# Performance work log

Measured on AMD Instinct MI355X. Metric: run time of the kernel, lower is better.

The kernel has to match this reference:

```python
import jax, jax.numpy as jnp
from jax import lax
import numpy as np

NEG_INF = -10000.0
MAX_W = 15          # max_span_width for every marker
M = 5               # num_markers
H = 1024            # encoder hidden size (deberta-v3-large)
B, N = 16, 2048


def _gelu(x):
    return jax.nn.gelu(x, approximate=False)  # torch nn.GELU default (erf)


def _consistency(scores, mask, gamma, width_logits):
    # scores: [B, N] token scores for one marker; mask: [B, N] int
    n = scores.shape[1]
    masked = jnp.where(mask == 0, NEG_INF, scores)
    ww = jax.nn.softmax(width_logits)  # [MAX_W]
    boosts = [masked]
    for w in range(2, min(MAX_W, n) + 1):
        # sliding-window min of width w -> span_mins [B, n-w+1]
        mins = lax.reduce_window(masked, float('inf'), lax.min,
                                 (1, w), (1, 1), 'VALID')
        weighted = mins * ww[w - 2]
        # expand each span-min back to every token it covers via sliding max
        p = jnp.pad(weighted, ((0, 0), (w - 1, w - 1)), constant_values=NEG_INF)
        expanded = lax.reduce_window(p, float('-inf'), lax.max,
                                     (1, w), (1, 1), 'VALID')  # [B, n]
        boosts.append(expanded)
    boost = jnp.max(jnp.stack(boosts, axis=0), axis=0)
    return scores + gamma * boost


def setup_inputs() -> dict:
    key = jax.random.key(0)
    ks = jax.random.split(key, 12)
    s = 0.02
    inp = {
        'h': jax.random.normal(ks[0], (B, N, H), jnp.float32),
        'attention_mask': jnp.ones((B, N), jnp.int32),
        # per-marker token scorers, stacked on leading marker axis
        'W1': jax.random.normal(ks[1], (M, H, 512), jnp.float32) * s,
        'b1': jnp.zeros((M, 512), jnp.float32),
        'W2': jax.random.normal(ks[2], (M, 512, 256), jnp.float32) * s,
        'b2': jnp.zeros((M, 256), jnp.float32),
        'W3': jax.random.normal(ks[3], (M, 256), jnp.float32) * s,
        'b3': jnp.zeros((M,), jnp.float32),
        # span-consistency params
        'gamma': jnp.ones((M,), jnp.float32),
        'width_logits': jax.random.normal(ks[4], (M, MAX_W), jnp.float32) * 0.1,
        # cross-marker attention params
        'corr': jnp.eye(M, dtype=jnp.float32) * 0.5,
        'cw1': jax.random.normal(ks[5], (M, 64), jnp.float32) * 0.1,
        'cb1': jnp.zeros((64,), jnp.float32),
        'cw2': jax.random.normal(ks[6], (64, M), jnp.float32) * 0.1,
        'cb2': jnp.zeros((M,), jnp.float32),
        'gate': jnp.array(0.3, jnp.float32),
    }
    return inp


def reference(h, attention_mask, W1, b1, W2, b2, W3, b3,
              gamma, width_logits, corr, cw1, cb1, cw2, cb2, gate):
    # token scorers (dropout is identity in eval): [M, B, N]
    t1 = _gelu(jnp.einsum('bnh,mhd->mbnd', h, W1) + b1[:, None, None, :])
    t2 = _gelu(jnp.einsum('mbnd,mde->mbne', t1, W2) + b2[:, None, None, :])
    scores = jnp.einsum('mbne,me->mbn', t2, W3) + b3[:, None, None]
    # per-marker span-consistency boost
    boosted = jax.vmap(_consistency, in_axes=(0, None, 0, 0))(
        scores, attention_mask, gamma, width_logits)      # [M, B, N]
    logits = jnp.transpose(boosted, (1, 2, 0))            # [B, N, M]
    # cross-marker attention
    probs = jax.nn.sigmoid(logits)
    correlated = probs @ corr
    refined = _gelu(correlated @ cw1 + cb1) @ cw2 + cb2
    return logits + jax.nn.sigmoid(gate) * refined
```

## Files before the change

kernel.cpp:

```cpp
#include <hip/hip_runtime.h>
#include <math.h>


typedef __bf16 bf16x8 __attribute__((ext_vector_type(8)));
typedef float f32x4 __attribute__((ext_vector_type(4)));

#define NEG_INF_VAL (-10000.0f)

__device__ __forceinline__ unsigned short f2bf(float f) {
  union { float f; unsigned u; } v; v.f = f;
  unsigned r = v.u + 0x7fffu + ((v.u >> 16) & 1u);
  return (unsigned short)(r >> 16);
}
__device__ __forceinline__ float bf2f(unsigned short b) {
  union { unsigned u; float f; } v; v.u = ((unsigned)b) << 16;
  return v.f;
}
__device__ __forceinline__ float gelu_erf(float x) {
  return 0.5f * x * (1.0f + erff(x * 0.7071067811865476f));
}
__device__ __forceinline__ float gelu_fast(float x) {
  float u = 0.7978845608f * x * (1.0f + 0.044715f * x * x);
  float e = __expf(-2.0f * fabsf(u));
  float t = (1.0f - e) / (1.0f + e);
  t = copysignf(t, u);
  return 0.5f * x * (1.0f + t);
}

__global__ __launch_bounds__(256) void k_f32_to_bf16x4(
    const float* __restrict__ in, unsigned short* __restrict__ out, int n4) {
  int i = blockIdx.x * 256 + threadIdx.x;
  if (i >= n4) return;
  float4 v = reinterpret_cast<const float4*>(in)[i];
  ushort4 o;
  o.x = f2bf(v.x); o.y = f2bf(v.y); o.z = f2bf(v.z); o.w = f2bf(v.w);
  reinterpret_cast<ushort4*>(out)[i] = o;
}

__global__ __launch_bounds__(256) void k_transpose_tiled(
    const float* __restrict__ W, unsigned short* __restrict__ Wt,
    int K, int C) {
  __shared__ float tile[32][33];
  const int m = blockIdx.z;
  const int c0 = blockIdx.x * 32, k0 = blockIdx.y * 32;
  const int tx = threadIdx.x & 31, ty = threadIdx.x >> 5;
  const float* Wm = W + (size_t)m * K * C;
#pragma unroll
  for (int r = ty; r < 32; r += 8)
    tile[r][tx] = Wm[(size_t)(k0 + r) * C + c0 + tx];
  __syncthreads();
  unsigned short* Wtm = Wt + (size_t)m * C * K;
#pragma unroll
  for (int r = ty; r < 32; r += 8)
    Wtm[(size_t)(c0 + r) * K + k0 + tx] = f2bf(tile[tx][r]);
}

#define STAGE(GP, LP)                                                        \
  __builtin_amdgcn_global_load_lds(                                          \
      (const __attribute__((address_space(1))) void*)(GP),                   \
      (__attribute__((address_space(3))) void*)(LP), 16, 0, 0)

#define TILE(SLOT, DO_S1, DO_S0, VM1, VM3)                                   \
  {                                                                          \
    bf16x8 af[4], bfr[4];                                                    \
                                               \
    _Pragma("unroll") for (int j = 0; j < 4; ++j)                            \
      bfr[j] = *reinterpret_cast<const bf16x8*>(                             \
          &Bs[SLOT][(wc * 4 + j) * 1024 + l8]);                              \
    _Pragma("unroll") for (int i = 0; i < 4; ++i)                            \
      af[i] = *reinterpret_cast<const bf16x8*>(                              \
          &As[SLOT][(wr * 8 + i) * 1024 + l8]);                              \
    if (DO_S1) {                                                             \
      STAGE(pA0 + 96, &As[1 - (SLOT)][(0 * 8 + w) * 1024 + 512 + l8]);       \
      STAGE(pA1 + 96, &As[1 - (SLOT)][(1 * 8 + w) * 1024 + 512 + l8]);       \
    }                                                                        \
    __builtin_amdgcn_s_barrier();                                            \
    __builtin_amdgcn_sched_barrier(0);                                       \
    asm volatile("s_waitcnt lgkmcnt(0)" ::: "memory");                       \
    __builtin_amdgcn_sched_barrier(0);                                       \
    __builtin_amdgcn_s_setprio(1);                                           \
    _Pragma("unroll") for (int i = 0; i < 4; ++i)                            \
      _Pragma("unroll") for (int j = 0; j < 4; ++j)                          \
        acc[i][j] = __builtin_amdgcn_mfma_f32_16x16x32_bf16(                 \
            af[i], bfr[j], acc[i][j], 0, 0, 0);                              \
    __builtin_amdgcn_s_setprio(0);                                           \
    __builtin_amdgcn_sched_barrier(0);                                       \
    __builtin_amdgcn_s_barrier();                                            \
    __builtin_amdgcn_sched_barrier(0);                                       \
                                               \
    _Pragma("unroll") for (int i = 0; i < 4; ++i)                            \
      af[i] = *reinterpret_cast<const bf16x8*>(                              \
          &As[SLOT][(wr * 8 + 4 + i) * 1024 + l8]);                          \
    if (DO_S1) {                                                             \
      STAGE(pB0 + 96, &Bs[1 - (SLOT)][(0 * 8 + w) * 1024 + 512 + l8]);       \
      STAGE(pB1 + 96, &Bs[1 - (SLOT)][(1 * 8 + w) * 1024 + 512 + l8]);       \
    }                                                                        \
    __builtin_amdgcn_s_barrier();                                            \
    __builtin_amdgcn_sched_barrier(0);                                       \
    asm volatile("s_waitcnt lgkmcnt(0)" ::: "memory");                       \
    __builtin_amdgcn_sched_barrier(0);                                       \
    __builtin_amdgcn_s_setprio(1);                                           \
    _Pragma("unroll") for (int i = 0; i < 4; ++i)                            \
      _Pragma("unroll") for (int j = 0; j < 4; ++j)                          \
        acc[4 + i][j] = __builtin_amdgcn_mfma_f32_16x16x32_bf16(             \
            af[i], bfr[j], acc[4 + i][j], 0, 0, 0);                          \
    __builtin_amdgcn_s_setprio(0);                                           \
    __builtin_amdgcn_sched_barrier(0);                                       \
    asm volatile("s_waitcnt vmcnt(" VM1 ")" ::: "memory");                   \
    __builtin_amdgcn_sched_barrier(0);                                       \
    __builtin_amdgcn_s_barrier();                                            \
    __builtin_amdgcn_sched_barrier(0);                                       \
                                               \
    _Pragma("unroll") for (int j = 0; j < 4; ++j)                            \
      bfr[j] = *reinterpret_cast<const bf16x8*>(                             \
          &Bs[SLOT][(wc * 4 + j) * 1024 + 512 + l8]);                        \
    _Pragma("unroll") for (int i = 0; i < 4; ++i)                            \
      af[i] = *reinterpret_cast<const bf16x8*>(                              \
          &As[SLOT][(wr * 8 + i) * 1024 + 512 + l8]);                        \
    if (DO_S0) {                                                             \
      STAGE(pA0 + 128, &As[SLOT][(0 * 8 + w) * 1024 + l8]);                  \
      STAGE(pA1 + 128, &As[SLOT][(1 * 8 + w) * 1024 + l8]);                  \
    }                                                                        \
    __builtin_amdgcn_s_barrier();                                            \
    __builtin_amdgcn_sched_barrier(0);                                       \
    asm volatile("s_waitcnt lgkmcnt(0)" ::: "memory");                       \
    __builtin_amdgcn_sched_barrier(0);                                       \
    __builtin_amdgcn_s_setprio(1);                                           \
    _Pragma("unroll") for (int i = 0; i < 4; ++i)                            \
      _Pragma("unroll") for (int j = 0; j < 4; ++j)                          \
        acc[i][j] = __builtin_amdgcn_mfma_f32_16x16x32_bf16(                 \
            af[i], bfr[j], acc[i][j], 0, 0, 0);                              \
    __builtin_amdgcn_s_setprio(0);                                           \
    __builtin_amdgcn_sched_barrier(0);                                       \
    __builtin_amdgcn_s_barrier();                                            \
    __builtin_amdgcn_sched_barrier(0);                                       \
                                               \
    _Pragma("unroll") for (int i = 0; i < 4; ++i)                            \
      af[i] = *reinterpret_cast<const bf16x8*>(                              \
          &As[SLOT][(wr * 8 + 4 + i) * 1024 + 512 + l8]);                    \
    if (DO_S0) {                                                             \
      STAGE(pB0 + 128, &Bs[SLOT][(0 * 8 + w) * 1024 + l8]);                  \
      STAGE(pB1 + 128, &Bs[SLOT][(1 * 8 + w) * 1024 + l8]);                  \
    }                                                                        \
    __builtin_amdgcn_s_barrier();                                            \
    __builtin_amdgcn_sched_barrier(0);                                       \
    asm volatile("s_waitcnt lgkmcnt(0)" ::: "memory");                       \
    __builtin_amdgcn_sched_barrier(0);                                       \
    __builtin_amdgcn_s_setprio(1);                                           \
    _Pragma("unroll") for (int i = 0; i < 4; ++i)                            \
      _Pragma("unroll") for (int j = 0; j < 4; ++j)                          \
        acc[4 + i][j] = __builtin_amdgcn_mfma_f32_16x16x32_bf16(             \
            af[i], bfr[j], acc[4 + i][j], 0, 0, 0);                          \
    __builtin_amdgcn_s_setprio(0);                                           \
    __builtin_amdgcn_sched_barrier(0);                                       \
    asm volatile("s_waitcnt vmcnt(" VM3 ")" ::: "memory");                   \
    __builtin_amdgcn_sched_barrier(0);                                       \
    __builtin_amdgcn_s_barrier();                                            \
    __builtin_amdgcn_sched_barrier(0);                                       \
    pA0 += 64; pA1 += 64; pB0 += 64; pB1 += 64;                              \
  }

template <bool FUSE_SCORES, int NT>
__global__ __launch_bounds__(512) void k_gemm256(
    const unsigned short* __restrict__ A, int lda, int aOffPerM,
    const unsigned short* __restrict__ Bt, int K,
    const float* __restrict__ bias,
    unsigned short* __restrict__ C, int ldc,
    const float* __restrict__ W3, const float* __restrict__ b3,
    float* __restrict__ scoresOut,
    int tilesPerM, int colsPerM, int nColTiles) {
  __shared__ __align__(16) unsigned short As[2][16384];
  __shared__ __align__(16) unsigned short Bs[2][16384];
  __shared__ float sc[256];
  const int t512 = threadIdx.x;
  const int w = t512 >> 6, l = t512 & 63;
  const int wr = w >> 2, wc = w & 3;
  const int l8 = l * 8;

  const int nwg = gridDim.x;
  const int cpx = nwg >> 3;
  const int bid = blockIdx.x;
  const int swz = (bid & 7) * cpx + (bid >> 3);
  const int ct = swz % nColTiles, rt = swz / nColTiles;
  const int m = ct / tilesPerM, cb = ct - m * tilesPerM;
  const int gcol0 = m * colsPerM + cb * 256;
  const int row0 = rt * 256;
  const unsigned short* Am = A + (size_t)m * aOffPerM;

  if (FUSE_SCORES && t512 < 256) sc[t512] = 0.f;

  f32x4 acc[8][4] = {};

  const int r = l & 15;
  const int c8 = (l >> 4) * 8;
  const unsigned short* pA0 = Am + (size_t)(row0 + w * 16 + r) * lda + c8;
  const unsigned short* pA1 = Am + (size_t)(row0 + 128 + w * 16 + r) * lda + c8;
  const unsigned short* pB0 = Bt + (size_t)(gcol0 + w * 16 + r) * (size_t)K + c8;
  const unsigned short* pB1 = Bt + (size_t)(gcol0 + 128 + w * 16 + r) * (size_t)K + c8;

  STAGE(pA0,      &As[0][(0 * 8 + w) * 1024 + l8]);
  STAGE(pA1,      &As[0][(1 * 8 + w) * 1024 + l8]);
  STAGE(pB0,      &Bs[0][(0 * 8 + w) * 1024 + l8]);
  STAGE(pB1,      &Bs[0][(1 * 8 + w) * 1024 + l8]);
  STAGE(pA0 + 32, &As[0][(0 * 8 + w) * 1024 + 512 + l8]);
  STAGE(pA1 + 32, &As[0][(1 * 8 + w) * 1024 + 512 + l8]);
  STAGE(pB0 + 32, &Bs[0][(0 * 8 + w) * 1024 + 512 + l8]);
  STAGE(pB1 + 32, &Bs[0][(1 * 8 + w) * 1024 + 512 + l8]);
  STAGE(pA0 + 64, &As[1][(0 * 8 + w) * 1024 + l8]);
  STAGE(pA1 + 64, &As[1][(1 * 8 + w) * 1024 + l8]);
  STAGE(pB0 + 64, &Bs[1][(0 * 8 + w) * 1024 + l8]);
  STAGE(pB1 + 64, &Bs[1][(1 * 8 + w) * 1024 + l8]);
  asm volatile("s_waitcnt vmcnt(8)" ::: "memory");
  __builtin_amdgcn_sched_barrier(0);
  __builtin_amdgcn_s_barrier();
  __builtin_amdgcn_sched_barrier(0);

#pragma unroll 1
  for (int t = 0; t < NT - 2; t += 2) {
    TILE(0, 1, 1, "8", "8");
    TILE(1, 1, 1, "8", "8");
  }
  TILE(0, 1, 0, "8", "4");
  TILE(1, 0, 0, "0", "0");

  if (!FUSE_SCORES) {
    const int orow = (l >> 4) * 4, ocol = l & 15;
#pragma unroll
    for (int i = 0; i < 8; ++i)
#pragma unroll
      for (int j = 0; j < 4; ++j) {
        const int gc = gcol0 + wc * 64 + j * 16 + ocol;
        const float bv = bias[gc];
        const int gr0 = row0 + wr * 128 + i * 16 + orow;
#pragma unroll
        for (int rr = 0; rr < 4; ++rr) {
          float v = gelu_fast(acc[i][j][rr] + bv);
          C[(size_t)(gr0 + rr) * ldc + gc] = f2bf(v);
        }
      }
  } else {
    const int ocol = l & 15;
#pragma unroll
    for (int i = 0; i < 8; ++i) {
      float rs[4] = {0.f, 0.f, 0.f, 0.f};
#pragma unroll
      for (int j = 0; j < 4; ++j) {
        const int cl = wc * 64 + j * 16 + ocol;
        const float bv = bias[m * 256 + cl];
        const float w3v = W3[m * 256 + cl];
#pragma unroll
        for (int rr = 0; rr < 4; ++rr)
          rs[rr] += gelu_fast(acc[i][j][rr] + bv) * w3v;
      }
#pragma unroll
      for (int s = 1; s < 16; s <<= 1)
#pragma unroll
        for (int rr = 0; rr < 4; ++rr)
          rs[rr] += __shfl_xor(rs[rr], s);
      if (ocol == 0) {
        const int lr0 = wr * 128 + i * 16 + (l >> 4) * 4;
#pragma unroll
        for (int rr = 0; rr < 4; ++rr)
          atomicAdd(&sc[lr0 + rr], rs[rr]);
      }
    }
    __syncthreads();
    if (t512 < 256)
      scoresOut[(size_t)m * 32768 + row0 + t512] = sc[t512] + b3[m];
  }
}

__global__ __launch_bounds__(256) void k_span(
    const float* __restrict__ scores,
    const int* __restrict__ mask,
    const float* __restrict__ gamma,
    const float* __restrict__ wlog,
    float* __restrict__ logits) {
  const int b = blockIdx.x, m = blockIdx.y;
  const int tid = threadIdx.x;
  __shared__ float masked[2048], mins[2048], boost[2048];
  __shared__ float ww[14];
  if (tid == 0) {
    float mx = -1e30f;
    for (int i = 0; i < 15; i++) mx = fmaxf(mx, wlog[m * 15 + i]);
    float e[15], sum = 0.f;
    for (int i = 0; i < 15; i++) { e[i] = expf(wlog[m * 15 + i] - mx); sum += e[i]; }
    for (int i = 0; i < 14; i++) ww[i] = e[i] / sum;
  }
  const float* srow = scores + ((size_t)m * 16 + b) * 2048;
  const int* mrow = mask + (size_t)b * 2048;
  for (int i = tid; i < 2048; i += 256) {
    float s = srow[i];
    float mk = (mrow[i] == 0) ? NEG_INF_VAL : s;
    masked[i] = mk; mins[i] = mk; boost[i] = mk;
  }
  __syncthreads();
  for (int w2 = 2; w2 <= 15; w2++) {
    for (int s = tid; s <= 2048 - w2; s += 256)
      mins[s] = fminf(mins[s], masked[s + w2 - 1]);
    __syncthreads();
    float c = ww[w2 - 2];
    for (int i = tid; i < 2048; i += 256) {
      int lo = i - w2 + 1; if (lo < 0) lo = 0;
      int hi = i; if (hi > 2048 - w2) hi = 2048 - w2;
      float mx = -1e30f;
      for (int s = lo; s <= hi; s++) mx = fmaxf(mx, mins[s]);
      boost[i] = fmaxf(boost[i], mx * c);
    }
    __syncthreads();
  }
  float g = gamma[m];
  for (int i = tid; i < 2048; i += 256)
    logits[((size_t)b * 2048 + i) * 5 + m] = srow[i] + g * boost[i];
}

__global__ __launch_bounds__(256) void k_cross(
    const float* __restrict__ logits, const float* __restrict__ corr,
    const float* __restrict__ cw1, const float* __restrict__ cb1,
    const float* __restrict__ cw2, const float* __restrict__ cb2,
    const float* __restrict__ gate, float* __restrict__ out) {
  __shared__ float s_corr[25], s_cw1[320], s_cb1[64], s_cw2[320], s_cb2[5];
  int tid = threadIdx.x;
  if (tid < 25) s_corr[tid] = corr[tid];
  if (tid < 64) s_cb1[tid] = cb1[tid];
  if (tid < 5)  s_cb2[tid] = cb2[tid];
  for (int i = tid; i < 320; i += 256) { s_cw1[i] = cw1[i]; s_cw2[i] = cw2[i]; }
  __syncthreads();
  int t = blockIdx.x * 256 + tid;
  float lg[5], pr[5];
#pragma unroll
  for (int m = 0; m < 5; m++) {
    lg[m] = logits[(size_t)t * 5 + m];
    pr[m] = 1.f / (1.f + expf(-lg[m]));
  }
  float co[5];
#pragma unroll
  for (int j = 0; j < 5; j++) {
    float s = 0.f;
#pragma unroll
    for (int mm = 0; mm < 5; mm++) s += pr[mm] * s_corr[mm * 5 + j];
    co[j] = s;
  }
  float ref[5];
#pragma unroll
  for (int m = 0; m < 5; m++) ref[m] = s_cb2[m];
  for (int k = 0; k < 64; k++) {
    float h = s_cb1[k];
#pragma unroll
    for (int j = 0; j < 5; j++) h += co[j] * s_cw1[j * 64 + k];
    h = gelu_erf(h);
#pragma unroll
    for (int m = 0; m < 5; m++) ref[m] += h * s_cw2[k * 5 + m];
  }
  float sg = 1.f / (1.f + expf(-gate[0]));
#pragma unroll
  for (int m = 0; m < 5; m++) out[(size_t)t * 5 + m] = lg[m] + sg * ref[m];
}

extern "C" void kernel_launch(void* const* d_in, const int* in_sizes, int n_in,
                              void* d_out, int out_size, void* d_ws, size_t ws_size,
                              hipStream_t stream) {
  const float* h     = (const float*)d_in[0];
  const int*   mask  = (const int*)d_in[1];
  const float* W1    = (const float*)d_in[2];
  const float* b1    = (const float*)d_in[3];
  const float* W2    = (const float*)d_in[4];
  const float* b2    = (const float*)d_in[5];
  const float* W3    = (const float*)d_in[6];
  const float* b3    = (const float*)d_in[7];
  const float* gamma = (const float*)d_in[8];
  const float* wlog  = (const float*)d_in[9];
  const float* corr  = (const float*)d_in[10];
  const float* cw1   = (const float*)d_in[11];
  const float* cb1   = (const float*)d_in[12];
  const float* cw2   = (const float*)d_in[13];
  const float* cb2   = (const float*)d_in[14];
  const float* gate  = (const float*)d_in[15];
  float* out = (float*)d_out;

  char* ws = (char*)d_ws;
  unsigned short* hb  = (unsigned short*)(ws);
  unsigned short* W1t = (unsigned short*)(ws + 67108864);
  unsigned short* W2t = (unsigned short*)(ws + 72351744);
  unsigned short* t1  = (unsigned short*)(ws + 73662464);
  float* scores       = (float*)(ws + 241434624);
  float* logits       = (float*)(ws + 242089984);

  k_f32_to_bf16x4<<<33554432 / 4 / 256, 256, 0, stream>>>(h, hb, 33554432 / 4);
  k_transpose_tiled<<<dim3(16, 32, 5), 256, 0, stream>>>(W1, W1t, 1024, 512);
  k_transpose_tiled<<<dim3(8, 16, 5), 256, 0, stream>>>(W2, W2t, 512, 256);

  k_gemm256<false, 16><<<1280, 512, 0, stream>>>(
      hb, 1024, 0, W1t, 1024, b1, t1, 2560,
      nullptr, nullptr, nullptr, 10, 2560, 10);
  k_gemm256<true, 8><<<640, 512, 0, stream>>>(
      t1, 2560, 512, W2t, 512, b2, nullptr, 0,
      W3, b3, scores, 1, 256, 5);

  k_span<<<dim3(16, 5), 256, 0, stream>>>(scores, mask, gamma, wlog, logits);
  k_cross<<<32768 / 256, 256, 0, stream>>>(logits, corr, cw1, cb1, cw2, cb2, gate, out);
}
```

Measured before the change: 681.5 us.

## Prefetch LDS fragments ahead with double register buffers and partial lgkmcnt waits

Restructures the inner GEMM tile loop so LDS fragment loads for the next MFMA phase are issued before the current phase's MFMAs. Double register buffers (afA/afB, bfrA/bfrB) and partial lgkmcnt waits in place of lgkmcnt(0) let LDS reads overlap matrix math. The vmcnt waits for global-to-LDS staging move to different points in the tile. This raises register pressure, and mistuned wait counts could introduce races on the staged LDS buffers.

New measurement: 666.4 us. -2.2%, faster.

```diff
diff --git a/kernel.cpp b/kernel.cpp
--- a/kernel.cpp
+++ b/kernel.cpp
@@ -60,103 +60,88 @@
       (const __attribute__((address_space(1))) void*)(GP),                   \
       (__attribute__((address_space(3))) void*)(LP), 16, 0, 0)
 
-#define TILE(SLOT, DO_S1, DO_S0, VM1, VM3)                                   \
+#define MFMA16(OFF, AF, BF)                                                  \
+    _Pragma("unroll") for (int i = 0; i < 4; ++i)                            \
+      _Pragma("unroll") for (int j = 0; j < 4; ++j)                          \
+        acc[(OFF) + i][j] = __builtin_amdgcn_mfma_f32_16x16x32_bf16(         \
+            AF[i], BF[j], acc[(OFF) + i][j], 0, 0, 0);
+
+#define BARRIER_PAIR()                                                       \
+    __builtin_amdgcn_sched_barrier(0);                                       \
+    __builtin_amdgcn_s_barrier();                                            \
+    __builtin_amdgcn_sched_barrier(0);
+
+#define TILE2(SLOT, DO_S1, DO_S0, VMQ0, VMQ3)                                \
   {                                                                          \
-    bf16x8 af[4], bfr[4];                                                    \
-                                               \
+    bf16x8 afA[4], afB[4], bfrA[4], bfrB[4];                                 \
+                                                           \
     _Pragma("unroll") for (int j = 0; j < 4; ++j)                            \
-      bfr[j] = *reinterpret_cast<const bf16x8*>(                             \
+      bfrA[j] = *reinterpret_cast<const bf16x8*>(                            \
           &Bs[SLOT][(wc * 4 + j) * 1024 + l8]);                              \
     _Pragma("unroll") for (int i = 0; i < 4; ++i)                            \
-      af[i] = *reinterpret_cast<const bf16x8*>(                              \
+      afA[i] = *reinterpret_cast<const bf16x8*>(                             \
           &As[SLOT][(wr * 8 + i) * 1024 + l8]);                              \
+    _Pragma("unroll") for (int i = 0; i < 4; ++i)                            \
+      afB[i] = *reinterpret_cast<const bf16x8*>(                             \
+          &As[SLOT][(wr * 8 + 4 + i) * 1024 + l8]);                          \
     if (DO_S1) {                                                             \
       STAGE(pA0 + 96, &As[1 - (SLOT)][(0 * 8 + w) * 1024 + 512 + l8]);       \
       STAGE(pA1 + 96, &As[1 - (SLOT)][(1 * 8 + w) * 1024 + 512 + l8]);       \
     }                                                                        \
-    __builtin_amdgcn_s_barrier();                                            \
-    __builtin_amdgcn_sched_barrier(0);                                       \
-    asm volatile("s_waitcnt lgkmcnt(0)" ::: "memory");                       \
+    asm volatile("s_waitcnt vmcnt(" VMQ0 ")" ::: "memory");                  \
+    BARRIER_PAIR();                                                          \
+    asm volatile("s_waitcnt lgkmcnt(4)" ::: "memory");                       \
     __builtin_amdgcn_sched_barrier(0);                                       \
     __builtin_amdgcn_s_setprio(1);                                           \
-    _Pragma("unroll") for (int i = 0; i < 4; ++i)                            \
-      _Pragma("unroll") for (int j = 0; j < 4; ++j)                          \
-        acc[i][j] = __builtin_amdgcn_mfma_f32_16x16x32_bf16(                 \
-            af[i], bfr[j], acc[i][j], 0, 0, 0);                              \
+    MFMA16(0, afA, bfrA);                                                    \
     __builtin_amdgcn_s_setprio(0);                                           \
-    __builtin_amdgcn_sched_barrier(0);                                       \
-    __builtin_amdgcn_s_barrier();                                            \
-    __builtin_amdgcn_sched_barrier(0);                                       \
-                                               \
-    _Pragma("unroll") for (int i = 0; i < 4; ++i)                            \
-      af[i] = *reinterpret_cast<const bf16x8*>(                              \
-          &As[SLOT][(wr * 8 + 4 + i) * 1024 + l8]);                          \
+    BARRIER_PAIR();                                                          \
+                                                           \
+    _Pragma("unroll") for (int j = 0; j < 4; ++j)                            \
+      bfrB[j] = *reinterpret_cast<const bf16x8*>(                            \
+          &Bs[SLOT][(wc * 4 + j) * 1024 + 512 + l8]);                        \
+    _Pragma("unroll") for (int i = 0; i < 4; ++i)                            \
+      afA[i] = *reinterpret_cast<const bf16x8*>(                             \
+          &As[SLOT][(wr * 8 + i) * 1024 + 512 + l8]);                        \
     if (DO_S1) {                                                             \
       STAGE(pB0 + 96, &Bs[1 - (SLOT)][(0 * 8 + w) * 1024 + 512 + l8]);       \
       STAGE(pB1 + 96, &Bs[1 - (SLOT)][(1 * 8 + w) * 1024 + 512 + l8]);       \
     }                                                                        \
-    __builtin_amdgcn_s_barrier();                                            \
-    __builtin_amdgcn_sched_barrier(0);                                       \
-    asm volatile("s_waitcnt lgkmcnt(0)" ::: "memory");                       \
+    BARRIER_PAIR();                                                          \
+    asm volatile("s_waitcnt lgkmcnt(8)" ::: "memory");                       \
     __builtin_amdgcn_sched_barrier(0);                                       \
     __builtin_amdgcn_s_setprio(1);                                           \
-    _Pragma("unroll") for (int i = 0; i < 4; ++i)                            \
-      _Pragma("unroll") for (int j = 0; j < 4; ++j)                          \
-        acc[4 + i][j] = __builtin_amdgcn_mfma_f32_16x16x32_bf16(             \
-            af[i], bfr[j], acc[4 + i][j], 0, 0, 0);                          \
+    MFMA16(4, afB, bfrA);                                                    \
     __builtin_amdgcn_s_setprio(0);                                           \
-    __builtin_amdgcn_sched_barrier(0);                                       \
-    asm volatile("s_waitcnt vmcnt(" VM1 ")" ::: "memory");                   \
-    __builtin_amdgcn_sched_barrier(0);                                       \
-    __builtin_amdgcn_s_barrier();                                            \
-    __builtin_amdgcn_sched_barrier(0);                                       \
-                                               \
-    _Pragma("unroll") for (int j = 0; j < 4; ++j)                            \
-      bfr[j] = *reinterpret_cast<const bf16x8*>(                             \
-          &Bs[SLOT][(wc * 4 + j) * 1024 + 512 + l8]);                        \
-    _Pragma("unroll") for (int i = 0; i < 4; ++i)                            \
-      af[i] = *reinterpret_cast<const bf16x8*>(                              \
-          &As[SLOT][(wr * 8 + i) * 1024 + 512 + l8]);                        \
+    BARRIER_PAIR();                                                          \
+                                                           \
+    _Pragma("unroll") for (int i = 0; i < 4; ++i)                            \
+      afB[i] = *reinterpret_cast<const bf16x8*>(                             \
+          &As[SLOT][(wr * 8 + 4 + i) * 1024 + 512 + l8]);                    \
     if (DO_S0) {                                                             \
       STAGE(pA0 + 128, &As[SLOT][(0 * 8 + w) * 1024 + l8]);                  \
       STAGE(pA1 + 128, &As[SLOT][(1 * 8 + w) * 1024 + l8]);                  \
     }                                                                        \
-    __builtin_amdgcn_s_barrier();                                            \
-    __builtin_amdgcn_sched_barrier(0);                                       \
-    asm volatile("s_waitcnt lgkmcnt(0)" ::: "memory");                       \
+    BARRIER_PAIR();                                                          \
+    asm volatile("s_waitcnt lgkmcnt(4)" ::: "memory");                       \
     __builtin_amdgcn_sched_barrier(0);                                       \
     __builtin_amdgcn_s_setprio(1);                                           \
-    _Pragma("unroll") for (int i = 0; i < 4; ++i)                            \
-      _Pragma("unroll") for (int j = 0; j < 4; ++j)                          \
-        acc[i][j] = __builtin_amdgcn_mfma_f32_16x16x32_bf16(                 \
-            af[i], bfr[j], acc[i][j], 0, 0, 0);                              \
+    MFMA16(0, afA, bfrB);                                                    \
     __builtin_amdgcn_s_setprio(0);                                           \
-    __builtin_amdgcn_sched_barrier(0);                                       \
-    __builtin_amdgcn_s_barrier();                                            \
-    __builtin_amdgcn_sched_barrier(0);                                       \
-                                               \
-    _Pragma("unroll") for (int i = 0; i < 4; ++i)                            \
-      af[i] = *reinterpret_cast<const bf16x8*>(                              \
-          &As[SLOT][(wr * 8 + 4 + i) * 1024 + 512 + l8]);                    \
+    BARRIER_PAIR();                                                          \
+                                                           \
     if (DO_S0) {                                                             \
       STAGE(pB0 + 128, &Bs[SLOT][(0 * 8 + w) * 1024 + l8]);                  \
       STAGE(pB1 + 128, &Bs[SLOT][(1 * 8 + w) * 1024 + l8]);                  \
     }                                                                        \
-    __builtin_amdgcn_s_barrier();                                            \
-    __builtin_amdgcn_sched_barrier(0);                                       \
+    asm volatile("s_waitcnt vmcnt(" VMQ3 ")" ::: "memory");                  \
+    BARRIER_PAIR();                                                          \
     asm volatile("s_waitcnt lgkmcnt(0)" ::: "memory");                       \
     __builtin_amdgcn_sched_barrier(0);                                       \
     __builtin_amdgcn_s_setprio(1);                                           \
-    _Pragma("unroll") for (int i = 0; i < 4; ++i)                            \
-      _Pragma("unroll") for (int j = 0; j < 4; ++j)                          \
-        acc[4 + i][j] = __builtin_amdgcn_mfma_f32_16x16x32_bf16(             \
-            af[i], bfr[j], acc[4 + i][j], 0, 0, 0);                          \
+    MFMA16(4, afB, bfrB);                                                    \
     __builtin_amdgcn_s_setprio(0);                                           \
-    __builtin_amdgcn_sched_barrier(0);                                       \
-    asm volatile("s_waitcnt vmcnt(" VM3 ")" ::: "memory");                   \
-    __builtin_amdgcn_sched_barrier(0);                                       \
-    __builtin_amdgcn_s_barrier();                                            \
-    __builtin_amdgcn_sched_barrier(0);                                       \
+    BARRIER_PAIR();                                                          \
     pA0 += 64; pA1 += 64; pB0 += 64; pB1 += 64;                              \
   }
 
@@ -211,17 +196,15 @@
   STAGE(pB0 + 64, &Bs[1][(0 * 8 + w) * 1024 + l8]);
   STAGE(pB1 + 64, &Bs[1][(1 * 8 + w) * 1024 + l8]);
   asm volatile("s_waitcnt vmcnt(8)" ::: "memory");
-  __builtin_amdgcn_sched_barrier(0);
-  __builtin_amdgcn_s_barrier();
-  __builtin_amdgcn_sched_barrier(0);
+  BARRIER_PAIR();
 
 #pragma unroll 1
   for (int t = 0; t < NT - 2; t += 2) {
-    TILE(0, 1, 1, "8", "8");
-    TILE(1, 1, 1, "8", "8");
-  }
-  TILE(0, 1, 0, "8", "4");
-  TILE(1, 0, 0, "0", "0");
+    TILE2(0, 1, 1, "6", "8");
+    TILE2(1, 1, 1, "6", "8");
+  }
+  TILE2(0, 1, 0, "6", "4");
+  TILE2(1, 0, 0, "0", "0");
 
   if (!FUSE_SCORES) {
     const int orow = (l >> 4) * 4, ocol = l & 15;
```
